# Performance work log

Measured on AMD Instinct MI355X. Metric: run time of the kernel, lower is better.

## Reference

```python
import jax, jax.numpy as jnp
import numpy as np

OFFSET = 1  # self.offset

def setup_inputs() -> dict:
    key = jax.random.key(0)
    k1, k2, k3, k4, k5 = jax.random.split(key, 5)
    B, D, T, S, N = 16, 512, 1024, 12, 10
    x = jax.random.normal(k1, (B, D, T), dtype=jnp.float32)
    y = jax.random.normal(k2, (B, D, T), dtype=jnp.float32)
    W = jax.random.normal(k3, (D, D, S), dtype=jnp.float32) * 0.05  # ConvTranspose2d weight [in, out, 1, steps] squeezed
    b = jax.random.normal(k4, (D,), dtype=jnp.float32) * 0.05
    neg_idxs = jax.random.randint(k5, (B, N * T), 0, T)
    return {"x": x, "y": y, "W": W, "b": b, "neg_idxs": neg_idxs}


def reference(x, y, W, b, neg_idxs):
    B, F, T = y.shape
    N = neg_idxs.shape[1] // T
    # --- sample_negatives: gather by computed index over flattened y ---
    y_flat = jnp.transpose(y, (1, 0, 2)).reshape(F, B * T)          # [F, B*T]
    idx = (neg_idxs + jnp.arange(B, dtype=neg_idxs.dtype)[:, None] * T).reshape(-1)
    negs = y_flat[:, idx].reshape(F, B, N, T).transpose(2, 1, 0, 3)  # [N, B, F, T]
    targets = jnp.concatenate([y[None], negs], axis=0)               # [C=N+1, B, F, T]
    # --- project_to_steps: ConvTranspose2d with kernel (1, steps) == per-step linear ---
    xp = jnp.einsum('bit,ios->bots', x, W) + b[None, :, None, None]  # [B, F, T, S]
    C = N + 1
    S = xp.shape[-1]
    steps = min(S, T - OFFSET)
    preds, labels = [], []
    for i in range(steps):  # small fixed loop over prediction steps
        off = i + OFFSET
        # [C, B, T-off]: dot over feature dim, copies broadcast over x
        p = jnp.einsum('bft,cbft->cbt', xp[:, :, :T - off, i], targets[:, :, :, off:])
        preds.append(p.reshape(-1))
        lab = jnp.zeros((C, B * (T - off)), dtype=xp.dtype).at[0].set(1.0)
        labels.append(lab.reshape(-1))
    predictions = jnp.concatenate(preds)
    labels_out = jnp.concatenate(labels)
    return predictions, labels_out
```

## Files before the change

### kernel.cpp

```cpp
#include <hip/hip_runtime.h>

typedef __bf16 bf16x8 __attribute__((ext_vector_type(8)));
typedef float f32x4 __attribute__((ext_vector_type(4)));

#define B_ 16
#define T_ 1024
#define D_ 512
#define S_ 12
#define C_ 11
static constexpr int P_TOTAL = 2148960;

__device__ __host__ inline constexpr int pred_base(int i) {
  return C_ * B_ * (T_ * i - (i * (i + 1)) / 2);
}

__device__ inline unsigned short f2bf(float f) {
  unsigned int u = __float_as_uint(f);
  u += 0x7FFF + ((u >> 16) & 1);
  return (unsigned short)(u >> 16);
}

__device__ inline void gld16(const void* g, void* l) {
  __builtin_amdgcn_global_load_lds(
      (const __attribute__((address_space(1))) void*)g,
      (__attribute__((address_space(3))) void*)l, 16, 0, 0);
}

__global__ __launch_bounds__(256) void prep_w(const float* __restrict__ W,
                                              unsigned short* __restrict__ wt) {
  __shared__ unsigned short tile[32][33][12];
  const int i0 = blockIdx.x * 32, o0 = blockIdx.y * 32;
#pragma unroll
  for (int q = 0; q < 48; ++q) {
    int idx = threadIdx.x + q * 256;
    int ii = idx / 384, rem = idx % 384;
    tile[ii][rem / 12][rem % 12] =
        f2bf(W[(size_t)(i0 + ii) * 6144 + (size_t)o0 * 12 + rem]);
  }
  __syncthreads();
#pragma unroll
  for (int q = 0; q < 48; ++q) {
    int idx = threadIdx.x + q * 256;
    int ss = idx / 1024, rem = idx % 1024;
    int oo = rem / 32, ii = rem % 32;
    wt[(size_t)ss * (D_ * D_) + (size_t)(o0 + oo) * D_ + (i0 + ii)] = tile[ii][oo][ss];
  }
}

__global__ __launch_bounds__(256) void prep_t2(const float* __restrict__ xin,
                                               const float* __restrict__ yin,
                                               unsigned short* __restrict__ xo,
                                               unsigned short* __restrict__ yo) {
  __shared__ float tile[32][33];
  const int t0 = blockIdx.x * 32;
  const int d0 = blockIdx.y * 32;
  const int b = blockIdx.z & 15;
  const float* in = (blockIdx.z < 16) ? xin : yin;
  unsigned short* ob = (blockIdx.z < 16) ? xo : yo;
  const float* ib = in + (size_t)b * D_ * T_;
  const int r = threadIdx.x / 32, c = threadIdx.x % 32;
#pragma unroll
  for (int p = 0; p < 4; ++p) {
    int rr = r + p * 8;
    tile[rr][c] = ib[(size_t)(d0 + rr) * T_ + t0 + c];
  }
  __syncthreads();
  unsigned short* op = ob + (size_t)b * T_ * D_;
#pragma unroll
  for (int p = 0; p < 4; ++p) {
    int rr = r + p * 8;
    op[(size_t)(t0 + rr) * D_ + d0 + c] = f2bf(tile[c][rr]);
  }
}

__global__ void labels_k(float* __restrict__ lab) {
  int k = blockIdx.x * 256 + threadIdx.x;
  if (k >= P_TOTAL) return;
  int i = 0;
#pragma unroll
  for (int q = 1; q < 12; ++q)
    if (k >= pred_base(q)) i = q;
  int rel = k - pred_base(i);
  int len = T_ - 1 - i;
  lab[k] = (rel < B_ * len) ? 1.0f : 0.0f;
}

__global__ __launch_bounds__(512, 1) void gemm_xp(
    const unsigned short* __restrict__ xb,
    const unsigned short* __restrict__ wt,
    const float* __restrict__ bias,
    unsigned short* __restrict__ xp,
    int tiles, int mtiles) {
  __shared__ char ldsb[131072];
  const int tid = threadIdx.x;
  const int w = tid >> 6, l = tid & 63;
  const int gm = w >> 2, gn = w & 3;
  const int fr = l & 15, sgrp = l >> 4;

  const int dox0 = tid * 16, dox1 = tid * 16 + 8192;
  const int rl0 = dox0 >> 7, rl1 = dox1 >> 7;
  const int col = dox0 & 127;
  const int sco0 = rl0 * 1024 + (col ^ ((rl0 & 7) << 4));
  const int sco1 = rl1 * 1024 + (col ^ ((rl1 & 7) << 4));

  auto stageH = [&](const char* panel, int ks, int half, int ldsBase) {
    const char* s = panel + half * 131072 + ks * 128;
    char* d = ldsb + ldsBase + half * 16384;
    gld16(s + sco0, d + dox0);
    gld16(s + sco1, d + dox1);
  };

  const int sw = (fr & 7) << 4;
  const int colk0 = (sgrp * 16) ^ sw;
  const int colk1 = (64 + sgrp * 16) ^ sw;
  const int aRowB = (gm * 64 + fr) * 128;
  const int bRowB = 32768 + (gn * 32 + fr) * 128;

  auto ldf = [&](int off) -> bf16x8 {
    return *(const bf16x8*)(ldsb + off);
  };

  auto decode = [&](int t, const unsigned short*& Ag, const unsigned short*& Bg,
                    int& n0v, int& miv, int& siv) {
    miv = t % mtiles;
    int rest = t / mtiles;
    int ni = rest & 1;
    siv = rest >> 1;
    Ag = xb + (size_t)(miv * 256) * D_;
    Bg = wt + ((size_t)siv * D_ + ni * 256) * D_;
    n0v = ni * 256;
  };

  int ti = blockIdx.x;
  if (ti >= tiles) return;
  const unsigned short *Ag, *Bg, *Agn = nullptr, *Bgn = nullptr;
  int n0, mi, si, n0n, min_, sin_;
  decode(ti, Ag, Bg, n0, mi, si);
  int tin = ti + gridDim.x;
  bool hasNext = tin < tiles;
  if (hasNext) decode(tin, Agn, Bgn, n0n, min_, sin_);

#define BAR()  asm volatile("" ::: "memory"); __builtin_amdgcn_s_barrier(); \
               asm volatile("" ::: "memory")

  stageH((const char*)Ag, 0, 0, 0);
  stageH((const char*)Bg, 0, 0, 32768);
  stageH((const char*)Ag, 0, 1, 0);
  stageH((const char*)Bg, 0, 1, 32768);
  asm volatile("s_waitcnt vmcnt(4)" ::: "memory");
  BAR();

  while (true) {
    f32x4 acc[8][4];
#pragma unroll
    for (int a = 0; a < 8; ++a)
#pragma unroll
      for (int bq = 0; bq < 4; ++bq)
#pragma unroll
        for (int e = 0; e < 4; ++e) acc[a][bq][e] = 0.f;

    float bv[2][2];
#pragma unroll
    for (int nh = 0; nh < 2; ++nh)
#pragma unroll
      for (int fn = 0; fn < 2; ++fn)
        bv[nh][fn] = bias[n0 + gn * 32 + nh * 128 + fn * 16 + fr];

#pragma unroll
    for (int ks = 0; ks < 8; ++ks) {
      const int bufB = (ks & 1) * 65536;
      const int nbufB = bufB ^ 65536;
      const bool st = (ks < 7) || hasNext;
      const char* pA = (ks < 7) ? (const char*)Ag : (const char*)Agn;
      const char* pB = (ks < 7) ? (const char*)Bg : (const char*)Bgn;
      const int kn = (ks < 7) ? ks + 1 : 0;
      bf16x8 af[2][4], b0[2][2], b1[2][2];

#pragma unroll
      for (int fm = 0; fm < 4; ++fm) {
        af[0][fm] = ldf(bufB + aRowB + fm * 2048 + colk0);
        af[1][fm] = ldf(bufB + aRowB + fm * 2048 + colk1);
      }
#pragma unroll
      for (int fn = 0; fn < 2; ++fn) {
        b0[0][fn] = ldf(bufB + bRowB + fn * 2048 + colk0);
        b0[1][fn] = ldf(bufB + bRowB + fn * 2048 + colk1);
      }
      if (st) {
        stageH(pA, kn, 0, nbufB);
        asm volatile("s_waitcnt vmcnt(2)" ::: "memory");
      } else {
        asm volatile("s_waitcnt vmcnt(0)" ::: "memory");
      }
      BAR();
      __builtin_amdgcn_s_setprio(1);
#pragma unroll
      for (int kk = 0; kk < 2; ++kk)
#pragma unroll
        for (int fm = 0; fm < 4; ++fm)
#pragma unroll
          for (int fn = 0; fn < 2; ++fn)
            acc[fm][fn] = __builtin_amdgcn_mfma_f32_16x16x32_bf16(
                af[kk][fm], b0[kk][fn], acc[fm][fn], 0, 0, 0);
      __builtin_amdgcn_s_setprio(0);
      BAR();

#pragma unroll
      for (int fn = 0; fn < 2; ++fn) {
        b1[0][fn] = ldf(bufB + bRowB + 16384 + fn * 2048 + colk0);
        b1[1][fn] = ldf(bufB + bRowB + 16384 + fn * 2048 + colk1);
      }
      if (st) stageH(pB, kn, 0, nbufB + 32768);
      BAR();
      __builtin_amdgcn_s_setprio(1);
#pragma unroll
      for (int kk = 0; kk < 2; ++kk)
#pragma unroll
        for (int fm = 0; fm < 4; ++fm)
#pragma unroll
          for (int fn = 0; fn < 2; ++fn)
            acc[fm][2 + fn] = __builtin_amdgcn_mfma_f32_16x16x32_bf16(
                af[kk][fm], b1[kk][fn], acc[fm][2 + fn], 0, 0, 0);
      __builtin_amdgcn_s_setprio(0);
      BAR();

#pragma unroll
      for (int fm = 0; fm < 4; ++fm) {
        af[0][fm] = ldf(bufB + aRowB + 16384 + fm * 2048 + colk0);
        af[1][fm] = ldf(bufB + aRowB + 16384 + fm * 2048 + colk1);
      }
      if (st) stageH(pA, kn, 1, nbufB);
      BAR();
      __builtin_amdgcn_s_setprio(1);
#pragma unroll
      for (int kk = 0; kk < 2; ++kk)
#pragma unroll
        for (int fm = 0; fm < 4; ++fm)
#pragma unroll
          for (int fn = 0; fn < 2; ++fn)
            acc[4 + fm][2 + fn] = __builtin_amdgcn_mfma_f32_16x16x32_bf16(
                af[kk][fm], b1[kk][fn], acc[4 + fm][2 + fn], 0, 0, 0);
      __builtin_amdgcn_s_setprio(0);
      BAR();

      if (st) stageH(pB, kn, 1, nbufB + 32768);
      BAR();
      __builtin_amdgcn_s_setprio(1);
#pragma unroll
      for (int kk = 0; kk < 2; ++kk)
#pragma unroll
        for (int fm = 0; fm < 4; ++fm)
#pragma unroll
          for (int fn = 0; fn < 2; ++fn)
            acc[4 + fm][fn] = __builtin_amdgcn_mfma_f32_16x16x32_bf16(
                af[kk][fm], b0[kk][fn], acc[4 + fm][fn], 0, 0, 0);
      __builtin_amdgcn_s_setprio(0);
      if (st) asm volatile("s_waitcnt vmcnt(4)" ::: "memory");
      BAR();
    }

#pragma unroll
    for (int mh = 0; mh < 2; ++mh) {
#pragma unroll
      for (int fm = 0; fm < 4; ++fm) {
#pragma unroll
        for (int r = 0; r < 4; ++r) {
          int m = mi * 256 + gm * 64 + mh * 128 + fm * 16 + sgrp * 4 + r;
          int bl = m >> 10, t = m & 1023;
          size_t orow = (((size_t)bl * S_ + si) * T_ + t) * D_;
#pragma unroll
          for (int nh = 0; nh < 2; ++nh)
#pragma unroll
            for (int fn = 0; fn < 2; ++fn) {
              int o = n0 + gn * 32 + nh * 128 + fn * 16 + fr;
              xp[orow + o] = f2bf(acc[mh * 4 + fm][nh * 2 + fn][r] + bv[nh][fn]);
            }
        }
      }
    }

    if (!hasNext) break;
    ti = tin;
    Ag = Agn; Bg = Bgn; n0 = n0n; mi = min_; si = sin_;
    tin = ti + gridDim.x;
    hasNext = tin < tiles;
    if (hasNext) decode(tin, Agn, Bgn, n0n, min_, sin_);
  }
#undef BAR
}

__global__ __launch_bounds__(256) void pred_k(
    const unsigned short* __restrict__ xp,
    const unsigned short* __restrict__ yT,
    const int* __restrict__ negs,
    float* __restrict__ preds, int b0) {
  const int w = threadIdx.x >> 6, l = threadIdx.x & 63;
  const int bl = blockIdx.y;
  const int b = b0 + bl;
  const int fr = l & 15;
  const int koff = (l >> 4) * 8;

  const unsigned short* arow[4];
  const unsigned short* brow[4];
  int tts[4];
#pragma unroll
  for (int q = 0; q < 4; ++q) {
    int tt = blockIdx.x * 4 + w + q * 256;
    tts[q] = tt;
    int t = tt - 1 - fr;
    bool av = (fr < S_) && (t >= 0);
    arow[q] = xp + (((size_t)bl * S_ + (av ? fr : 0)) * T_ + (av ? t : 0)) * D_;
    int j = tt;
    if (fr >= 1 && fr <= 10) j = negs[b * (10 * T_) + (fr - 1) * T_ + tt];
    brow[q] = yT + ((size_t)b * T_ + j) * D_;
  }

  f32x4 acc[4];
#pragma unroll
  for (int q = 0; q < 4; ++q)
#pragma unroll
    for (int e = 0; e < 4; ++e) acc[q][e] = 0.f;

#pragma unroll
  for (int kk = 0; kk < 16; ++kk) {
#pragma unroll
    for (int q = 0; q < 4; ++q) {
      bf16x8 a = *(const bf16x8*)(arow[q] + kk * 32 + koff);
      bf16x8 bb = *(const bf16x8*)(brow[q] + kk * 32 + koff);
      acc[q] = __builtin_amdgcn_mfma_f32_16x16x32_bf16(a, bb, acc[q], 0, 0, 0);
    }
  }

#pragma unroll
  for (int q = 0; q < 4; ++q) {
#pragma unroll
    for (int r = 0; r < 4; ++r) {
      int ii = (l >> 4) * 4 + r;
      int to = tts[q] - 1 - ii;
      if (ii < S_ && fr < C_ && tts[q] >= 1 && to >= 0) {
        int len = T_ - 1 - ii;
        preds[pred_base(ii) + ((size_t)fr * B_ + b) * len + to] = acc[q][r];
      }
    }
  }
}

extern "C" void kernel_launch(void* const* d_in, const int* in_sizes, int n_in,
                              void* d_out, int out_size, void* d_ws, size_t ws_size,
                              hipStream_t stream) {
  (void)in_sizes; (void)n_in; (void)out_size;
  const float* x = (const float*)d_in[0];
  const float* y = (const float*)d_in[1];
  const float* W = (const float*)d_in[2];
  const float* bias = (const float*)d_in[3];
  const int* negs = (const int*)d_in[4];
  float* out = (float*)d_out;
  char* ws = (char*)d_ws;

  unsigned short* wt = (unsigned short*)ws;
  unsigned short* xb = (unsigned short*)(ws + 6291456);
  unsigned short* yT = (unsigned short*)(ws + 6291456 + 16777216);
  unsigned short* xp = (unsigned short*)(ws + 6291456 + 2 * 16777216);
  const size_t fixed = 6291456 + (size_t)2 * 16777216;
  const size_t xp_per_b = (size_t)S_ * T_ * D_ * 2;
  int nb = 1;
  if (ws_size > fixed) {
    size_t cap = (ws_size - fixed) / xp_per_b;
    nb = cap < 1 ? 1 : (cap > 16 ? 16 : (int)cap);
  }

  hipLaunchKernelGGL(prep_w, dim3(16, 16), dim3(256), 0, stream, W, wt);
  hipLaunchKernelGGL(prep_t2, dim3(32, 16, 32), dim3(256), 0, stream, x, y, xb, yT);
  hipLaunchKernelGGL(labels_k, dim3((P_TOTAL + 255) / 256), dim3(256), 0, stream,
                     out + P_TOTAL);

  for (int b0 = 0; b0 < B_; b0 += nb) {
    int bc = (B_ - b0) < nb ? (B_ - b0) : nb;
    int tiles = bc * 4 * 2 * 12;
    int grid = tiles < 256 ? tiles : 256;
    hipLaunchKernelGGL(gemm_xp, dim3(grid), dim3(512), 0, stream,
                       xb + (size_t)b0 * T_ * D_, wt, bias, xp,
                       tiles, bc * 4);
    hipLaunchKernelGGL(pred_k, dim3(64, bc), dim3(256), 0, stream,
                       xp, yT, negs, out, b0);
  }
}
```

Measured before the change: 211.6 us.

## Stage GEMM epilogue through LDS for coalesced 16-byte xp stores

The xp GEMM epilogue used to write scattered 2-byte bf16 stores straight to global memory. It now packs bias-added results as bf16 pairs into a swizzled LDS stash, then writes each 128-row half with 16-byte vectorized stores. To make those adjacent-column pairs line up, the K-dimension element order in both the transposed-input and weight prep kernels is permuted consistently, which changes the in-register column mapping. This adds barriers and LDS traffic in the epilogue in exchange for far fewer, wider global stores.

Result: slower. 239.9 us (+13.4%).

```diff
diff --git a/kernel.cpp b/kernel.cpp
--- a/kernel.cpp
+++ b/kernel.cpp
@@ -1,7 +1,9 @@
 #include <hip/hip_runtime.h>
 
 typedef __bf16 bf16x8 __attribute__((ext_vector_type(8)));
+typedef __bf16 bf16x2 __attribute__((ext_vector_type(2)));
 typedef float f32x4 __attribute__((ext_vector_type(4)));
+typedef unsigned int u32x4 __attribute__((ext_vector_type(4)));
 
 #define B_ 16
 #define T_ 1024
@@ -20,6 +22,8 @@
   return (unsigned short)(u >> 16);
 }
 
+__device__ inline int perm5(int v) { return ((v & 15) << 1) | (v >> 4); }
+
 __device__ inline void gld16(const void* g, void* l) {
   __builtin_amdgcn_global_load_lds(
       (const __attribute__((address_space(1))) void*)g,
@@ -43,7 +47,8 @@
     int idx = threadIdx.x + q * 256;
     int ss = idx / 1024, rem = idx % 1024;
     int oo = rem / 32, ii = rem % 32;
-    wt[(size_t)ss * (D_ * D_) + (size_t)(o0 + oo) * D_ + (i0 + ii)] = tile[ii][oo][ss];
+    wt[(size_t)ss * (D_ * D_) + (size_t)(o0 + oo) * D_ + i0 + perm5(ii)] =
+        tile[ii][oo][ss];
   }
 }
 
@@ -69,7 +74,7 @@
 #pragma unroll
   for (int p = 0; p < 4; ++p) {
     int rr = r + p * 8;
-    op[(size_t)(t0 + rr) * D_ + d0 + c] = f2bf(tile[c][rr]);
+    op[(size_t)(t0 + rr) * D_ + d0 + perm5(c)] = f2bf(tile[c][rr]);
   }
 }
 
@@ -259,24 +264,43 @@
       BAR();
     }
 
-#pragma unroll
-    for (int mh = 0; mh < 2; ++mh) {
-#pragma unroll
-      for (int fm = 0; fm < 4; ++fm) {
-#pragma unroll
-        for (int r = 0; r < 4; ++r) {
-          int m = mi * 256 + gm * 64 + mh * 128 + fm * 16 + sgrp * 4 + r;
+    {
+      const int stashB = 65536;
+#pragma unroll
+      for (int mh = 0; mh < 2; ++mh) {
+        if (mh) { BAR(); }
+#pragma unroll
+        for (int fm = 0; fm < 4; ++fm) {
+#pragma unroll
+          for (int r = 0; r < 4; ++r) {
+            const int m_loc = gm * 64 + fm * 16 + sgrp * 4 + r;
+            const int sw2 = ((m_loc >> 2) & 3) << 2;
+#pragma unroll
+            for (int nh = 0; nh < 2; ++nh) {
+              bf16x2 pk;
+              pk[0] = (__bf16)(acc[mh * 4 + fm][nh * 2 + 0][r] + bv[nh][0]);
+              pk[1] = (__bf16)(acc[mh * 4 + fm][nh * 2 + 1][r] + bv[nh][1]);
+              const int colp = (nh * 64 + gn * 16 + fr) ^ sw2;
+              *(bf16x2*)(ldsb + stashB + (m_loc * 128 + colp) * 4) = pk;
+            }
+          }
+        }
+        BAR();
+#pragma unroll
+        for (int q = 0; q < 8; ++q) {
+          int id = tid + q * 512;
+          int m_loc = id >> 5;
+          int chk = id & 31;
+          int chkp = chk ^ ((m_loc >> 2) & 3);
+          u32x4 v = *(const u32x4*)(ldsb + stashB + m_loc * 512 + chkp * 16);
+          int m = mi * 256 + mh * 128 + m_loc;
           int bl = m >> 10, t = m & 1023;
-          size_t orow = (((size_t)bl * S_ + si) * T_ + t) * D_;
-#pragma unroll
-          for (int nh = 0; nh < 2; ++nh)
-#pragma unroll
-            for (int fn = 0; fn < 2; ++fn) {
-              int o = n0 + gn * 32 + nh * 128 + fn * 16 + fr;
-              xp[orow + o] = f2bf(acc[mh * 4 + fm][nh * 2 + fn][r] + bv[nh][fn]);
-            }
+          char* dst = (char*)xp +
+              (((((size_t)bl * S_ + si) * T_ + t) * D_) + n0) * 2 + chk * 16;
+          *(u32x4*)dst = v;
         }
       }
+      BAR();
     }
 
     if (!hasNext) break;
```
